# Kernel tuning notes

Hardware: AMD Instinct MI355X
Metric: run time of the kernel (lower is better)

Reference implementation:

```python
import jax, jax.numpy as jnp
import numpy as np

B, T, CIN, COUT, E, K = 2000, 32, 32, 128, 32000, 2
NEG = 0.01  # LeakyReLU default negative slope
EPS = 1e-5


def setup_inputs() -> dict:
    key = jax.random.key(0)
    ks = jax.random.split(key, 8)
    x = jax.random.normal(ks[0], (B, CIN, T), dtype=jnp.float32)
    edge_index = jax.random.randint(ks[1], (2, E), 0, B, dtype=jnp.int32)
    edge_weight = jax.random.uniform(ks[2], (E,), dtype=jnp.float32)
    conv_w = jax.random.normal(ks[3], (COUT, CIN, 3), dtype=jnp.float32) * 0.1
    conv_b = jnp.zeros((COUT,), dtype=jnp.float32)
    ln_gamma = jnp.ones((COUT, T), dtype=jnp.float32)
    ln_beta = jnp.zeros((COUT, T), dtype=jnp.float32)
    tag_w = jax.random.normal(ks[4], (K + 1, COUT, COUT), dtype=jnp.float32) * 0.05
    tag_b = jnp.zeros((COUT,), dtype=jnp.float32)
    return {"x": x, "edge_index": edge_index, "edge_weight": edge_weight,
            "conv_w": conv_w, "conv_b": conv_b, "ln_gamma": ln_gamma,
            "ln_beta": ln_beta, "tag_w": tag_w, "tag_b": tag_b}


def leaky_relu(x):
    return jnp.where(x >= 0, x, NEG * x)


def reference(x, edge_index, edge_weight, conv_w, conv_b, ln_gamma, ln_beta, tag_w, tag_b):
    # --- Temporal1DConvLayer: causal conv1d (pad k-1 then truncate to T) + LeakyReLU ---
    y = jax.lax.conv_general_dilated(
        x, conv_w, window_strides=(1,), padding=[(2, 0)],
        dimension_numbers=("NCH", "OIH", "NCH"))  # [B, COUT, T]
    y = y + conv_b[None, :, None]
    y = leaky_relu(y)  # pool='none', norm=Identity inside temporal layer

    # --- temporal LayerNorm over [COUT, T] ---
    mu = jnp.mean(y, axis=(1, 2), keepdims=True)
    var = jnp.var(y, axis=(1, 2), keepdims=True)
    y = (y - mu) * jax.lax.rsqrt(var + EPS) * ln_gamma[None] + ln_beta[None]

    # --- reshape to time-parallel node features [T*B, COUT] ---
    xp = jnp.transpose(y, (2, 0, 1)).reshape(T * B, COUT)

    # --- replicate edges per timestep with node-offset t*B ---
    offs = (jnp.arange(T, dtype=edge_index.dtype) * B)[:, None]  # [T,1]
    src = (edge_index[0][None, :] + offs).reshape(-1)  # [T*E]
    dst = (edge_index[1][None, :] + offs).reshape(-1)
    w = jnp.tile(edge_weight, T)
    N = T * B

    # --- TAGConv gcn normalization ---
    deg = jax.ops.segment_sum(w, dst, num_segments=N)
    dis = jnp.where(deg > 0, jax.lax.rsqrt(jnp.maximum(deg, 1e-12)), 0.0)
    norm = dis[src] * w * dis[dst]

    # --- k-hop propagation: out = sum_k A_norm^k x @ W_k + b ---
    out = xp @ tag_w[0]
    h = xp
    for k in range(1, K + 1):
        h = jax.ops.segment_sum(norm[:, None] * h[src], dst, num_segments=N)
        out = out + h @ tag_w[k]
    out = out + tag_b[None, :]

    # --- residual + activation (ResidualLayer 'res+') ---
    h_out = xp + leaky_relu(out)

    # --- back to [B, COUT, T] ---
    return jnp.transpose(h_out.reshape(T, B, COUT), (1, 2, 0))
```

## Files before the change

### kernel.cpp

```cpp
#include <hip/hip_runtime.h>
#include <hip/hip_bf16.h>
#include <math.h>

#define B_N   2000
#define T_N   32
#define CIN_N 32
#define COUT_N 128
#define E_N   32000
#define NEG_S 0.01f
#define EPS_S 1e-5f
#define NNODE (B_N * T_N)
#define EPAD_N 38016
#define META_I4 21009

typedef __attribute__((ext_vector_type(8))) __bf16 bf16x8;
typedef __attribute__((ext_vector_type(4))) float f32x4;
typedef __attribute__((ext_vector_type(2))) float f32x2;
typedef __attribute__((ext_vector_type(8))) unsigned short u16x8;

__device__ __forceinline__ unsigned short f2bf(float f) {
  unsigned u = __builtin_bit_cast(unsigned, f);
  u += 0x7FFFu + ((u >> 16) & 1u);
  return (unsigned short)(u >> 16);
}
__device__ __forceinline__ float bf2f(unsigned short h) {
  unsigned u = ((unsigned)h) << 16;
  return __builtin_bit_cast(float, u);
}

__global__ __launch_bounds__(256) void k_prep(
    const float* __restrict__ cw, const float* __restrict__ tw,
    unsigned short* __restrict__ wBc, unsigned short* __restrict__ wB,
    int4* __restrict__ meta)
{
  const int tid0 = blockIdx.x * 256 + threadIdx.x;
  const int stride = gridDim.x * 256;
  const int4 z = {0, 0, 0, 0};
  for (int i = tid0; i < META_I4; i += stride) meta[i] = z;
  for (int idx = tid0; idx < 12288; idx += stride) {
    int e = idx & 7, lane = (idx >> 3) & 63, rest = idx >> 9;
    int ks = rest % 3, nf2 = rest / 3;
    int col = nf2 * 16 + (lane & 15);
    int k = ks * 32 + ((lane >> 4) << 3) + e;
    wBc[idx] = f2bf(cw[col * 96 + k]);
  }
  for (int idx = tid0; idx < 49152; idx += stride) {
    int e = idx & 7, lane = (idx >> 3) & 63, rest = idx >> 9;
    int ks = rest % 12, nf2 = rest / 12;
    int col = nf2 * 16 + (lane & 15);
    int k = ks * 32 + ((lane >> 4) << 3) + e;
    wB[idx] = f2bf(tw[(k >> 7) * 16384 + (k & 127) * 128 + col]);
  }
}

__global__ __launch_bounds__(512, 4) void k_convln(
    const float* __restrict__ x, const unsigned short* __restrict__ wBc,
    const float* __restrict__ cb, const float* __restrict__ gamma,
    const float* __restrict__ beta, unsigned short* __restrict__ x0)
{
  __shared__ unsigned short sB[12288];
  __shared__ float sx4[4][1088];
  __shared__ float red1[8], red2[8];
  const int tid = threadIdx.x;
  const int w = tid >> 6, lane = tid & 63;
  const int s = w >> 1;
  const int b = blockIdx.x * 4 + s;
  const int t0 = (w & 1) * 16;
  const int r = lane & 15, q = lane >> 4;

  #pragma unroll
  for (int i = 0; i < 3; ++i) {
    int id = i * 512 + tid;
    ((float4*)sB)[id] = ((const float4*)wBc)[id];
  }
  for (int idx = tid; idx < 4 * 1088; idx += 512) {
    int ss = idx / 1088;
    int rem = idx - ss * 1088;
    int ci = rem / 34, tt = rem - ci * 34;
    sx4[ss][rem] = (tt >= 2) ? x[(blockIdx.x * 4 + ss) * 1024 + ci * 32 + (tt - 2)] : 0.f;
  }
  __syncthreads();

  const int ta = t0 + r;
  u16x8 a_[3];
  #pragma unroll
  for (int ks = 0; ks < 3; ++ks) {
    #pragma unroll
    for (int e = 0; e < 8; ++e) {
      int k = ks * 32 + q * 8 + e;
      int ci = k / 3, kk = k - ci * 3;
      a_[ks][e] = f2bf(sx4[s][ci * 34 + ta + kk]);
    }
  }

  f32x4 acc[8] = {};
  #pragma unroll
  for (int ks = 0; ks < 3; ++ks) {
    bf16x8 a = __builtin_bit_cast(bf16x8, a_[ks]);
    #pragma unroll
    for (int nf = 0; nf < 8; ++nf) {
      bf16x8 bv = *(const bf16x8*)&sB[((nf * 3 + ks) * 64 + lane) * 8];
      acc[nf] = __builtin_amdgcn_mfma_f32_16x16x32_bf16(a, bv, acc[nf], 0, 0, 0);
    }
  }

  float s1 = 0.f, s2 = 0.f;
  #pragma unroll
  for (int nf = 0; nf < 8; ++nf) {
    const float bias = cb[nf * 16 + r];
    #pragma unroll
    for (int i = 0; i < 4; ++i) {
      float u = acc[nf][i] + bias;
      u = (u >= 0.f) ? u : NEG_S * u;
      acc[nf][i] = u;
      s1 += u; s2 += u * u;
    }
  }
  #pragma unroll
  for (int d = 32; d > 0; d >>= 1) {
    s1 += __shfl_down(s1, d);
    s2 += __shfl_down(s2, d);
  }
  if (lane == 0) { red1[w] = s1; red2[w] = s2; }
  __syncthreads();
  const float a1 = red1[w & ~1] + red1[w | 1];
  const float a2 = red2[w & ~1] + red2[w | 1];
  const float mu = a1 / 4096.f;
  const float rs = rsqrtf(a2 / 4096.f - mu * mu + EPS_S);

  #pragma unroll
  for (int nf = 0; nf < 8; ++nf) {
    const int col = nf * 16 + r;
    #pragma unroll
    for (int i = 0; i < 4; ++i) {
      const int t = t0 + q * 4 + i;
      float v = (acc[nf][i] - mu) * rs * gamma[col * 32 + t] + beta[col * 32 + t];
      x0[((size_t)b * 32 + t) * 128 + col] = f2bf(v);
    }
  }
}

__global__ void k_deg(const int* __restrict__ ei, const float* __restrict__ ew,
                      float* __restrict__ deg, int* __restrict__ cnt)
{
  int e = blockIdx.x * 256 + threadIdx.x;
  if (e >= E_N) return;
  int d = ei[E_N + e];
  atomicAdd(&deg[d], ew[e]);
  atomicAdd(&cnt[d], 1);
}

__global__ __launch_bounds__(256) void k_scan(const int* __restrict__ cnt, int* __restrict__ offs)
{
  __shared__ int wsum[4];
  int tid = threadIdx.x;
  int vals[8];
  int run = 0;
  #pragma unroll
  for (int i = 0; i < 8; ++i) {
    int idx = tid * 8 + i;
    vals[i] = run;
    int v = (idx < B_N) ? cnt[idx] : 0;
    v = (v + 3) & ~3;
    run += v;
  }
  int lane = tid & 63, wid = tid >> 6;
  int xs = run;
  #pragma unroll
  for (int d = 1; d < 64; d <<= 1) {
    int y = __shfl_up(xs, d);
    if (lane >= d) xs += y;
  }
  if (lane == 63) wsum[wid] = xs;
  __syncthreads();
  int pre = 0;
  for (int w = 0; w < wid; ++w) pre += wsum[w];
  int excl = pre + xs - run;
  #pragma unroll
  for (int i = 0; i < 8; ++i) {
    int idx = tid * 8 + i;
    if (idx <= B_N) offs[idx] = excl + vals[i];
  }
}

__global__ void k_scatter(const int* __restrict__ ei, const float* __restrict__ ew,
                          const float* __restrict__ deg, const int* __restrict__ offs,
                          int* __restrict__ cursor, int* __restrict__ csr_src,
                          float* __restrict__ csr_norm)
{
  int e = blockIdx.x * 256 + threadIdx.x;
  if (e >= E_N) return;
  int s = ei[e], d = ei[E_N + e];
  float ds_ = deg[s], dd = deg[d];
  float dis_s = (ds_ > 0.f) ? rsqrtf(fmaxf(ds_, 1e-12f)) : 0.f;
  float dis_d = (dd  > 0.f) ? rsqrtf(fmaxf(dd,  1e-12f)) : 0.f;
  float nrm = dis_s * ew[e] * dis_d;
  int pos = offs[d] + atomicAdd(&cursor[d], 1);
  csr_src[pos] = s;
  csr_norm[pos] = nrm;
}

__global__ __launch_bounds__(256) void k_prop(
    const unsigned short* __restrict__ hin, unsigned short* __restrict__ hout,
    const int* __restrict__ offs, const int* __restrict__ csr_src,
    const float* __restrict__ csr_norm)
{
  const int bid = blockIdx.x;
  const int tq = bid & 7;
  const int bgroup = bid >> 3;
  const int widx = threadIdx.x >> 6;
  const int lane = threadIdx.x & 63;
  const int b = bgroup * 4 + widx;
  int beg = offs[b], end = offs[b + 1];
  const size_t lelem = (size_t)(tq * 4 + (lane >> 4)) * 128 + (lane & 15) * 8;
  const uint4* hp = (const uint4*)hin;
  const size_t lvec = lelem >> 3;

  f32x2 acc2[4] = {};
  for (int i = beg; i < end; i += 4) {
    int4   s4 = *(const int4*)&csr_src[i];
    float4 n4 = *(const float4*)&csr_norm[i];
    uint4 w0 = hp[(size_t)s4.x * 512 + lvec];
    uint4 w1 = hp[(size_t)s4.y * 512 + lvec];
    uint4 w2 = hp[(size_t)s4.z * 512 + lvec];
    uint4 w3 = hp[(size_t)s4.w * 512 + lvec];
    const unsigned ua[4][4] = {{w0.x, w0.y, w0.z, w0.w}, {w1.x, w1.y, w1.z, w1.w},
                               {w2.x, w2.y, w2.z, w2.w}, {w3.x, w3.y, w3.z, w3.w}};
    const float nm[4] = {n4.x, n4.y, n4.z, n4.w};
    #pragma unroll
    for (int e = 0; e < 4; ++e) {
      f32x2 nn; nn.x = nm[e]; nn.y = nm[e];
      #pragma unroll
      for (int p = 0; p < 4; ++p) {
        f32x2 f;
        f.x = __builtin_bit_cast(float, ua[e][p] << 16);
        f.y = __builtin_bit_cast(float, ua[e][p] & 0xFFFF0000u);
        acc2[p] += nn * f;
      }
    }
  }
  u16x8 o;
  #pragma unroll
  for (int p = 0; p < 4; ++p) {
    o[2 * p]     = f2bf(acc2[p].x);
    o[2 * p + 1] = f2bf(acc2[p].y);
  }
  *(u16x8*)&hout[(size_t)b * 4096 + lelem] = o;
}

__global__ __launch_bounds__(512, 4) void k_gemm(
    const unsigned short* __restrict__ x0, const unsigned short* __restrict__ h1,
    const unsigned short* __restrict__ h2, const unsigned short* __restrict__ wB,
    const float* __restrict__ tb, float* __restrict__ out)
{
  __shared__ unsigned short sB[24576];
  const int tid = threadIdx.x;
  const int w = tid >> 6, lane = tid & 63;
  const int sel = blockIdx.x / 250;
  const int b = (blockIdx.x % 250) * 8 + w;
  const int thalf = sel & 1, chalf = sel >> 1;
  const int t0 = thalf * 16;
  const int r = lane & 15, q = lane >> 4;

  const size_t abase = ((size_t)b * 32 + t0 + r) * 128 + q * 8;
  bf16x8 a[12];
  #pragma unroll
  for (int ks = 0; ks < 12; ++ks) {
    const unsigned short* arr = (ks < 4) ? x0 : (ks < 8) ? h1 : h2;
    a[ks] = *(const bf16x8*)&arr[abase + (size_t)(ks & 3) * 32];
  }

  const float4* gB = (const float4*)(wB + (size_t)chalf * 24576);
  #pragma unroll
  for (int i = 0; i < 6; ++i) {
    int id = i * 512 + tid;
    ((float4*)sB)[id] = gB[id];
  }
  __syncthreads();

  f32x4 acc[4] = {};
  #pragma unroll
  for (int ks = 0; ks < 12; ++ks) {
    #pragma unroll
    for (int nf = 0; nf < 4; ++nf) {
      bf16x8 bv = *(const bf16x8*)&sB[((nf * 12 + ks) * 64 + lane) * 8];
      acc[nf] = __builtin_amdgcn_mfma_f32_16x16x32_bf16(a[ks], bv, acc[nf], 0, 0, 0);
    }
  }

  #pragma unroll
  for (int nf = 0; nf < 4; ++nf) {
    const int col = chalf * 64 + nf * 16 + r;
    const float bias = tb[col];
    float4 o;
    #pragma unroll
    for (int i = 0; i < 4; ++i) {
      const int t = t0 + q * 4 + i;
      float u = acc[nf][i] + bias;
      u = (u >= 0.f) ? u : NEG_S * u;
      float xv = bf2f(x0[((size_t)b * 32 + t) * 128 + col]);
      ((float*)&o)[i] = xv + u;
    }
    *(float4*)&out[(size_t)b * 4096 + col * 32 + t0 + q * 4] = o;
  }
}

extern "C" void kernel_launch(void* const* d_in, const int* in_sizes, int n_in,
                              void* d_out, int out_size, void* d_ws, size_t ws_size,
                              hipStream_t stream)
{
  const float* x     = (const float*)d_in[0];
  const int*   ei    = (const int*)d_in[1];
  const float* ew    = (const float*)d_in[2];
  const float* cw    = (const float*)d_in[3];
  const float* cb    = (const float*)d_in[4];
  const float* gamma = (const float*)d_in[5];
  const float* beta  = (const float*)d_in[6];
  const float* tw    = (const float*)d_in[7];
  const float* tb    = (const float*)d_in[8];
  float* out = (float*)d_out;

  unsigned short* x0 = (unsigned short*)d_ws;
  unsigned short* h1 = x0 + (size_t)NNODE * 128;
  unsigned short* h2 = h1 + (size_t)NNODE * 128;
  float* deg = (float*)(h2 + (size_t)NNODE * 128);
  int*   cnt    = (int*)(deg + B_N);
  int*   cursor = cnt + B_N;
  int*   offs   = cursor + B_N;
  int*   csr_src = offs + (B_N + 4);
  float* csr_norm = (float*)(csr_src + EPAD_N);
  unsigned short* wBc = (unsigned short*)(csr_norm + EPAD_N);
  unsigned short* wB  = wBc + 12288;

  k_prep<<<96, 256, 0, stream>>>(cw, tw, wBc, wB, (int4*)deg);
  k_convln<<<500, 512, 0, stream>>>(x, wBc, cb, gamma, beta, x0);
  k_deg<<<(E_N + 255) / 256, 256, 0, stream>>>(ei, ew, deg, cnt);
  k_scan<<<1, 256, 0, stream>>>(cnt, offs);
  k_scatter<<<(E_N + 255) / 256, 256, 0, stream>>>(ei, ew, deg, offs, cursor, csr_src, csr_norm);
  k_prop<<<4000, 256, 0, stream>>>(x0, h1, offs, csr_src, csr_norm);
  k_prop<<<4000, 256, 0, stream>>>(h1, h2, offs, csr_src, csr_norm);
  k_gemm<<<1000, 512, 0, stream>>>(x0, h1, h2, wB, tb, out);
}
```

Baseline: 106.8 us.

## Pack CSR src and bf16 norm into one word; loop column halves in GEMM

The CSR edge list now stores the source index and a bf16-rounded normalization weight in a single 32-bit word, so each propagation step loads half as much edge metadata. The GEMM kernel now loops over both column halves within one block instead of splitting them across blocks, so the A operand (x0, h1, h2 fragments) is loaded once and reused for both halves. This halves the GEMM grid and adds an extra LDS reload and barrier per block. Rounding the edge norm to bf16 reduces precision, and the 16-bit source index relies on there being fewer than 65536 nodes.

```diff
diff --git a/kernel.cpp b/kernel.cpp
--- a/kernel.cpp
+++ b/kernel.cpp
@@ -11,7 +11,7 @@
 #define EPS_S 1e-5f
 #define NNODE (B_N * T_N)
 #define EPAD_N 38016
-#define META_I4 21009
+#define META_I4 11505
 
 typedef __attribute__((ext_vector_type(8))) __bf16 bf16x8;
 typedef __attribute__((ext_vector_type(4))) float f32x4;
@@ -185,8 +185,7 @@
 
 __global__ void k_scatter(const int* __restrict__ ei, const float* __restrict__ ew,
                           const float* __restrict__ deg, const int* __restrict__ offs,
-                          int* __restrict__ cursor, int* __restrict__ csr_src,
-                          float* __restrict__ csr_norm)
+                          int* __restrict__ cursor, unsigned* __restrict__ csr_pk)
 {
   int e = blockIdx.x * 256 + threadIdx.x;
   if (e >= E_N) return;
@@ -196,14 +195,12 @@
   float dis_d = (dd  > 0.f) ? rsqrtf(fmaxf(dd,  1e-12f)) : 0.f;
   float nrm = dis_s * ew[e] * dis_d;
   int pos = offs[d] + atomicAdd(&cursor[d], 1);
-  csr_src[pos] = s;
-  csr_norm[pos] = nrm;
+  csr_pk[pos] = ((unsigned)f2bf(nrm) << 16) | (unsigned)s;
 }
 
 __global__ __launch_bounds__(256) void k_prop(
     const unsigned short* __restrict__ hin, unsigned short* __restrict__ hout,
-    const int* __restrict__ offs, const int* __restrict__ csr_src,
-    const float* __restrict__ csr_norm)
+    const int* __restrict__ offs, const unsigned* __restrict__ csr_pk)
 {
   const int bid = blockIdx.x;
   const int tq = bid & 7;
@@ -218,15 +215,17 @@
 
   f32x2 acc2[4] = {};
   for (int i = beg; i < end; i += 4) {
-    int4   s4 = *(const int4*)&csr_src[i];
-    float4 n4 = *(const float4*)&csr_norm[i];
-    uint4 w0 = hp[(size_t)s4.x * 512 + lvec];
-    uint4 w1 = hp[(size_t)s4.y * 512 + lvec];
-    uint4 w2 = hp[(size_t)s4.z * 512 + lvec];
-    uint4 w3 = hp[(size_t)s4.w * 512 + lvec];
+    uint4 pk = *(const uint4*)&csr_pk[i];
+    uint4 w0 = hp[(size_t)(pk.x & 0xFFFFu) * 512 + lvec];
+    uint4 w1 = hp[(size_t)(pk.y & 0xFFFFu) * 512 + lvec];
+    uint4 w2 = hp[(size_t)(pk.z & 0xFFFFu) * 512 + lvec];
+    uint4 w3 = hp[(size_t)(pk.w & 0xFFFFu) * 512 + lvec];
     const unsigned ua[4][4] = {{w0.x, w0.y, w0.z, w0.w}, {w1.x, w1.y, w1.z, w1.w},
                                {w2.x, w2.y, w2.z, w2.w}, {w3.x, w3.y, w3.z, w3.w}};
-    const float nm[4] = {n4.x, n4.y, n4.z, n4.w};
+    const float nm[4] = {__builtin_bit_cast(float, pk.x & 0xFFFF0000u),
+                         __builtin_bit_cast(float, pk.y & 0xFFFF0000u),
+                         __builtin_bit_cast(float, pk.z & 0xFFFF0000u),
+                         __builtin_bit_cast(float, pk.w & 0xFFFF0000u)};
     #pragma unroll
     for (int e = 0; e < 4; ++e) {
       f32x2 nn; nn.x = nm[e]; nn.y = nm[e];
@@ -256,9 +255,8 @@
   __shared__ unsigned short sB[24576];
   const int tid = threadIdx.x;
   const int w = tid >> 6, lane = tid & 63;
-  const int sel = blockIdx.x / 250;
+  const int thalf = blockIdx.x / 250;
   const int b = (blockIdx.x % 250) * 8 + w;
-  const int thalf = sel & 1, chalf = sel >> 1;
   const int t0 = thalf * 16;
   const int r = lane & 15, q = lane >> 4;
 
@@ -270,38 +268,41 @@
     a[ks] = *(const bf16x8*)&arr[abase + (size_t)(ks & 3) * 32];
   }
 
-  const float4* gB = (const float4*)(wB + (size_t)chalf * 24576);
-  #pragma unroll
-  for (int i = 0; i < 6; ++i) {
-    int id = i * 512 + tid;
-    ((float4*)sB)[id] = gB[id];
-  }
-  __syncthreads();
-
-  f32x4 acc[4] = {};
-  #pragma unroll
-  for (int ks = 0; ks < 12; ++ks) {
+  for (int chalf = 0; chalf < 2; ++chalf) {
+    if (chalf) __syncthreads();
+    const float4* gB = (const float4*)(wB + (size_t)chalf * 24576);
+    #pragma unroll
+    for (int i = 0; i < 6; ++i) {
+      int id = i * 512 + tid;
+      ((float4*)sB)[id] = gB[id];
+    }
+    __syncthreads();
+
+    f32x4 acc[4] = {};
+    #pragma unroll
+    for (int ks = 0; ks < 12; ++ks) {
+      #pragma unroll
+      for (int nf = 0; nf < 4; ++nf) {
+        bf16x8 bv = *(const bf16x8*)&sB[((nf * 12 + ks) * 64 + lane) * 8];
+        acc[nf] = __builtin_amdgcn_mfma_f32_16x16x32_bf16(a[ks], bv, acc[nf], 0, 0, 0);
+      }
+    }
+
     #pragma unroll
     for (int nf = 0; nf < 4; ++nf) {
-      bf16x8 bv = *(const bf16x8*)&sB[((nf * 12 + ks) * 64 + lane) * 8];
-      acc[nf] = __builtin_amdgcn_mfma_f32_16x16x32_bf16(a[ks], bv, acc[nf], 0, 0, 0);
-    }
-  }
-
-  #pragma unroll
-  for (int nf = 0; nf < 4; ++nf) {
-    const int col = chalf * 64 + nf * 16 + r;
-    const float bias = tb[col];
-    float4 o;
-    #pragma unroll
-    for (int i = 0; i < 4; ++i) {
-      const int t = t0 + q * 4 + i;
-      float u = acc[nf][i] + bias;
-      u = (u >= 0.f) ? u : NEG_S * u;
-      float xv = bf2f(x0[((size_t)b * 32 + t) * 128 + col]);
-      ((float*)&o)[i] = xv + u;
-    }
-    *(float4*)&out[(size_t)b * 4096 + col * 32 + t0 + q * 4] = o;
+      const int col = chalf * 64 + nf * 16 + r;
+      const float bias = tb[col];
+      float4 o;
+      #pragma unroll
+      for (int i = 0; i < 4; ++i) {
+        const int t = t0 + q * 4 + i;
+        float u = acc[nf][i] + bias;
+        u = (u >= 0.f) ? u : NEG_S * u;
+        float xv = bf2f(x0[((size_t)b * 32 + t) * 128 + col]);
+        ((float*)&o)[i] = xv + u;
+      }
+      *(float4*)&out[(size_t)b * 4096 + col * 32 + t0 + q * 4] = o;
+    }
   }
 }
 
@@ -327,17 +328,16 @@
   int*   cnt    = (int*)(deg + B_N);
   int*   cursor = cnt + B_N;
   int*   offs   = cursor + B_N;
-  int*   csr_src = offs + (B_N + 4);
-  float* csr_norm = (float*)(csr_src + EPAD_N);
-  unsigned short* wBc = (unsigned short*)(csr_norm + EPAD_N);
+  unsigned* csr_pk = (unsigned*)(offs + (B_N + 4));
+  unsigned short* wBc = (unsigned short*)(csr_pk + EPAD_N);
   unsigned short* wB  = wBc + 12288;
 
   k_prep<<<96, 256, 0, stream>>>(cw, tw, wBc, wB, (int4*)deg);
   k_convln<<<500, 512, 0, stream>>>(x, wBc, cb, gamma, beta, x0);
   k_deg<<<(E_N + 255) / 256, 256, 0, stream>>>(ei, ew, deg, cnt);
   k_scan<<<1, 256, 0, stream>>>(cnt, offs);
-  k_scatter<<<(E_N + 255) / 256, 256, 0, stream>>>(ei, ew, deg, offs, cursor, csr_src, csr_norm);
-  k_prop<<<4000, 256, 0, stream>>>(x0, h1, offs, csr_src, csr_norm);
-  k_prop<<<4000, 256, 0, stream>>>(h1, h2, offs, csr_src, csr_norm);
-  k_gemm<<<1000, 512, 0, stream>>>(x0, h1, h2, wB, tb, out);
-}
+  k_scatter<<<(E_N + 255) / 256, 256, 0, stream>>>(ei, ew, deg, offs, cursor, csr_pk);
+  k_prop<<<4000, 256, 0, stream>>>(x0, h1, offs, csr_pk);
+  k_prop<<<4000, 256, 0, stream>>>(h1, h2, offs, csr_pk);
+  k_gemm<<<500, 512, 0, stream>>>(x0, h1, h2, wB, tb, out);
+}
```

Result: faster. 101.3 us (-5.1%).
